# Optimization experiments

Measured on AMD Instinct MI355X. Metric: run time of the kernel, lower is better.

Reference implementation:

```python
import jax, jax.numpy as jnp
import numpy as np

STEPS = 16      # max ICP iterations (module init arg `steps`)
TOL = 1e-6      # convergence tolerance (module init arg `tol`)


def _sqdist(a, b):
    # a: [B,N,3], b: [B,M,3] -> squared Euclidean distances [B,N,M] via GEMM
    a2 = jnp.sum(a * a, axis=-1)            # [B,N]
    b2 = jnp.sum(b * b, axis=-1)            # [B,M]
    ab = jnp.einsum('bnd,bmd->bnm', a, b)   # [B,N,M]
    return jnp.maximum(a2[..., :, None] + b2[..., None, :] - 2.0 * ab, 0.0)


def _kabsch(src, tgt):
    # Rigid transform (R, t) minimizing ||R*src + t - tgt|| via 3x3 SVD (svdtf)
    cs = src.mean(axis=-2, keepdims=True)   # [B,1,3]
    ct = tgt.mean(axis=-2, keepdims=True)
    H = jnp.einsum('bni,bnj->bij', src - cs, tgt - ct)  # [B,3,3]
    U, S, Vt = jnp.linalg.svd(H)
    V = jnp.swapaxes(Vt, -1, -2)
    Ut = jnp.swapaxes(U, -1, -2)
    d = jnp.linalg.det(V @ Ut)              # [B], reflection fix
    D = (jnp.zeros_like(H)
         .at[..., 0, 0].set(1.0)
         .at[..., 1, 1].set(1.0)
         .at[..., 2, 2].set(d))
    R = V @ D @ Ut                          # [B,3,3]
    t = ct[..., 0, :] - jnp.einsum('bij,bj->bi', R, cs[..., 0, :])  # [B,3]
    return R, t


def _icp(source, target):
    B = source.shape[0]

    def step(carry, _):
        temporal, errlast, done = carry
        d2 = _sqdist(temporal, target)                      # [B,N,M]
        knnidx = jnp.argmin(d2, axis=-1)                    # [B,N] 1-NN indices
        knnd2 = jnp.take_along_axis(d2, knnidx[..., None], axis=-1)[..., 0]
        errnew = jnp.sqrt(knnd2).mean(axis=-1)              # [B]
        # early-exit: once all batch errors converged, freeze state (emulates break)
        done = done | jnp.all(jnp.abs(errnew - errlast) < TOL)
        knntgt = jnp.take_along_axis(target, knnidx[..., None], axis=-2)  # [B,N,3]
        R, t = _kabsch(temporal, knntgt)
        new_temporal = jnp.einsum('bij,bnj->bni', R, temporal) + t[:, None, :]
        temporal = jnp.where(done, temporal, new_temporal)
        errlast = jnp.where(done, errlast, errnew)
        return (temporal, errlast, done), None

    init = (source, jnp.zeros((B,), source.dtype), jnp.array(False))
    (temporal, _, _), _ = jax.lax.scan(step, init, None, length=STEPS)
    # final transform from original source to aligned cloud (svdtf(source, temporal))
    R, t = _kabsch(source, temporal)
    return jnp.concatenate([R, t[..., None]], axis=-1)    # [B,3,4] = [R | t]


def setup_inputs() -> dict:
    key = jax.random.key(0)
    k1, k2 = jax.random.split(key)
    source = jax.random.normal(k1, (4, 4096, 3), dtype=jnp.float32)
    target = jax.random.normal(k2, (4, 4096, 3), dtype=jnp.float32)
    return {"source": source, "target": target}


def reference(source, target):
    return _icp(source, target)
```

## Files before the change

### kernel.cpp

```cpp
#include <hip/hip_runtime.h>

#define BATCH   4
#define NPTS    4096
#define MPTS    4096
#define NSTEPS  16
#define ICP_TOL 1e-6f

#define TPB        512
#define NBLOCKS    256
#define BLK_PER_B  64

#define ACC_OFF 0
#define CNT_OFF 65536
#define MST_OFF 69632
#define ZERO_DWORDS ((CNT_OFF + 4096) / 4)

typedef float v2f __attribute__((ext_vector_type(2)));


__device__ inline void normalize3f(float v[3]) {
    float n2 = v[0]*v[0] + v[1]*v[1] + v[2]*v[2];
    float inv = (n2 > 1e-30f) ? (1.0f / sqrtf(n2)) : 0.0f;
    v[0] *= inv; v[1] *= inv; v[2] *= inv;
}

__device__ inline void cross3f(const float a[3], const float b[3], float c[3]) {
    c[0] = a[1]*b[2] - a[2]*b[1];
    c[1] = a[2]*b[0] - a[0]*b[2];
    c[2] = a[0]*b[1] - a[1]*b[0];
}

__device__ inline void eigvec_f32(const float K[3][3], float la, float lb, float v[3]) {
    float A[3][3], Bm[3][3], C[3][3];
    #pragma unroll
    for (int i = 0; i < 3; i++)
        #pragma unroll
        for (int j = 0; j < 3; j++) {
            A[i][j]  = K[i][j] - ((i == j) ? la : 0.0f);
            Bm[i][j] = K[i][j] - ((i == j) ? lb : 0.0f);
        }
    #pragma unroll
    for (int i = 0; i < 3; i++)
        #pragma unroll
        for (int j = 0; j < 3; j++) {
            float s = 0.0f;
            #pragma unroll
            for (int k = 0; k < 3; k++) s += A[i][k] * Bm[k][j];
            C[i][j] = s;
        }
    int best = 0; float bn = -1.0f;
    #pragma unroll
    for (int c = 0; c < 3; c++) {
        float n2 = C[0][c]*C[0][c] + C[1][c]*C[1][c] + C[2][c]*C[2][c];
        if (n2 > bn) { bn = n2; best = c; }
    }
    if (bn > 1e-28f) {
        float inv = 1.0f / sqrtf(bn);
        v[0] = C[0][best]*inv; v[1] = C[1][best]*inv; v[2] = C[2][best]*inv;
    } else {
        v[0] = 1.0f; v[1] = 0.0f; v[2] = 0.0f;
    }
}

__device__ inline void kabsch_f32(const double S[16], float R[3][3], float t[3]) {
    const double inv_n = 1.0 / (double)NPTS;
    float cs[3] = { (float)(S[0]*inv_n), (float)(S[1]*inv_n), (float)(S[2]*inv_n) };
    float ct[3] = { (float)(S[3]*inv_n), (float)(S[4]*inv_n), (float)(S[5]*inv_n) };
    float H[3][3];
    #pragma unroll
    for (int i = 0; i < 3; i++)
        #pragma unroll
        for (int j = 0; j < 3; j++)
            H[i][j] = (float)(S[6 + 3*i + j] - S[i]*S[3 + j]*inv_n);

    float K[3][3];
    #pragma unroll
    for (int i = 0; i < 3; i++)
        #pragma unroll
        for (int j = 0; j < 3; j++) {
            float s = 0.0f;
            #pragma unroll
            for (int k = 0; k < 3; k++) s += H[k][i]*H[k][j];
            K[i][j] = s;
        }

    float q = (K[0][0] + K[1][1] + K[2][2]) * (1.0f/3.0f);
    float p1 = K[0][1]*K[0][1] + K[0][2]*K[0][2] + K[1][2]*K[1][2];
    float a00 = K[0][0]-q, a11 = K[1][1]-q, a22 = K[2][2]-q;
    float p2 = a00*a00 + a11*a11 + a22*a22 + 2.0f*p1;
    float p = sqrtf(p2 * (1.0f/6.0f));
    float l1, l2, l3;
    if (p < 1e-18f) {
        l1 = l2 = l3 = q;
    } else {
        float ip = 1.0f / p;
        float b00 = a00*ip, b01 = K[0][1]*ip, b02 = K[0][2]*ip;
        float b11 = a11*ip, b12 = K[1][2]*ip, b22 = a22*ip;
        float detB = b00*(b11*b22 - b12*b12)
                   - b01*(b01*b22 - b12*b02)
                   + b02*(b01*b12 - b11*b02);
        float r = 0.5f * detB;
        r = fminf(fmaxf(r, -1.0f), 1.0f);
        float phi = acosf(r) * (1.0f/3.0f);
        l1 = q + 2.0f*p*cosf(phi);
        l3 = q + 2.0f*p*cosf(phi + 2.0943951f);
        l2 = 3.0f*q - l1 - l3;
    }

    float v1[3], v2[3], v3[3];
    eigvec_f32(K, l2, l3, v1);
    eigvec_f32(K, l1, l3, v2);
    float d12 = v1[0]*v2[0] + v1[1]*v2[1] + v1[2]*v2[2];
    #pragma unroll
    for (int i = 0; i < 3; i++) v2[i] -= d12*v1[i];
    normalize3f(v2);
    cross3f(v1, v2, v3);

    float u1[3], u2[3], u3[3];
    #pragma unroll
    for (int i = 0; i < 3; i++) u1[i] = H[i][0]*v1[0] + H[i][1]*v1[1] + H[i][2]*v1[2];
    normalize3f(u1);
    #pragma unroll
    for (int i = 0; i < 3; i++) u2[i] = H[i][0]*v2[0] + H[i][1]*v2[1] + H[i][2]*v2[2];
    float du = u1[0]*u2[0] + u1[1]*u2[1] + u1[2]*u2[2];
    #pragma unroll
    for (int i = 0; i < 3; i++) u2[i] -= du*u1[i];
    normalize3f(u2);
    cross3f(u1, u2, u3);

    #pragma unroll
    for (int i = 0; i < 3; i++)
        #pragma unroll
        for (int j = 0; j < 3; j++)
            R[i][j] = v1[i]*u1[j] + v2[i]*u2[j] + v3[i]*u3[j];
    #pragma unroll
    for (int i = 0; i < 3; i++)
        t[i] = ct[i] - (R[i][0]*cs[0] + R[i][1]*cs[1] + R[i][2]*cs[2]);
}


__global__ void k_init(unsigned int* __restrict__ wsz) {
    int i = blockIdx.x * blockDim.x + threadIdx.x;
    if (i < ZERO_DWORDS) wsz[i] = 0u;
}

__global__ __launch_bounds__(TPB, 2)
void k_icp(const float* __restrict__ src, const float* __restrict__ tgt,
           double* __restrict__ accD, unsigned int* __restrict__ cntU,
           float* __restrict__ MstF) {
    __shared__ __align__(16) float Xs[MPTS];
    __shared__ __align__(16) float Ys[MPTS];
    __shared__ __align__(16) float Zs[MPTS];
    __shared__ __align__(16) float Ws[MPTS];
    __shared__ double pmem[8][16];
    __shared__ double Ssh[16];
    __shared__ float  Rsh[14];

    const int bid  = blockIdx.x;
    const int b    = bid >> 6;
    const int lb   = bid & (BLK_PER_B - 1);
    const int tid  = threadIdx.x;
    const int w    = tid >> 6;
    const int lane = tid & 63;

    const float* tgb = tgt + (size_t)b * MPTS * 3;
    const float* spb = src + ((size_t)b * NPTS + lb * 64 + w * 8) * 3;

    for (int i = tid; i < MPTS; i += TPB) {
        float x = tgb[3*i], y = tgb[3*i+1], z = tgb[3*i+2];
        Xs[i] = x; Ys[i] = y; Zs[i] = z;
        Ws[i] = 0.5f*(x*x + y*y + z*z);
    }

    float px[8], py[8], pz[8];
    #pragma unroll
    for (int k = 0; k < 8; k++) {
        px[k] = spb[3*k+0]; py[k] = spb[3*k+1]; pz[k] = spb[3*k+2];
    }
    float m00=1.f,m01=0.f,m02=0.f, m10=0.f,m11=1.f,m12=0.f, m20=0.f,m21=0.f,m22=1.f;
    float mt0=0.f,mt1=0.f,mt2=0.f;
    __syncthreads();

    const v2f* Xv = (const v2f*)Xs;
    const v2f* Yv = (const v2f*)Ys;
    const v2f* Zv = (const v2f*)Zs;
    const v2f* Wv = (const v2f*)Ws;

    for (int s = 0; s < NSTEPS; ++s) {
        v2f nx[8], ny[8], nz[8];
        #pragma unroll
        for (int k = 0; k < 8; k++) {
            nx[k] = (v2f){-px[k], -px[k]};
            ny[k] = (v2f){-py[k], -py[k]};
            nz[k] = (v2f){-pz[k], -pz[k]};
        }
        float bs[8]; int bm[8];
        #pragma unroll
        for (int k = 0; k < 8; k++) { bs[k] = 1e30f; bm[k] = 0; }

        #pragma unroll 4
        for (int j = 0; j < (MPTS/2)/64; ++j) {
            int q = (j << 6) | lane;
            v2f Xp = Xv[q], Yp = Yv[q], Zp = Zv[q], Wp = Wv[q];
            #pragma unroll
            for (int k = 0; k < 8; k++) {
                v2f f0, f1, f2;
                asm("v_pk_fma_f32 %0, %1, %2, %3" : "=v"(f0) : "v"(nx[k]), "v"(Xp), "v"(Wp));
                asm("v_pk_fma_f32 %0, %1, %2, %3" : "=v"(f1) : "v"(ny[k]), "v"(Yp), "v"(f0));
                asm("v_pk_fma_f32 %0, %1, %2, %3" : "=v"(f2) : "v"(nz[k]), "v"(Zp), "v"(f1));
                float lo = f2.x, hi = f2.y;
                float bsn = fminf(fminf(lo, hi), bs[k]);
                int ip = (q << 1) | ((hi < lo) ? 1 : 0);
                bm[k] = (bsn < bs[k]) ? ip : bm[k];
                bs[k] = bsn;
            }
        }
        #pragma unroll
        for (int off = 32; off >= 1; off >>= 1) {
            #pragma unroll
            for (int k = 0; k < 8; k++) {
                float os = __shfl_xor(bs[k], off);
                int   om = __shfl_xor(bm[k], off);
                if (os < bs[k] || (os == bs[k] && om < bm[k])) { bs[k] = os; bm[k] = om; }
            }
        }
        if (lane == 0) {
            double acc[16];
            #pragma unroll
            for (int i = 0; i < 16; i++) acc[i] = 0.0;
            #pragma unroll
            for (int k = 0; k < 8; k++) {
                int mm = bm[k];
                float qx = Xs[mm], qy = Ys[mm], qz = Zs[mm];
                float a2 = px[k]*px[k] + py[k]*py[k] + pz[k]*pz[k];
                float d2 = fmaxf(a2 + 2.0f*bs[k], 0.0f);
                double pxd = px[k], pyd = py[k], pzd = pz[k];
                double qxd = qx, qyd = qy, qzd = qz;
                acc[0] += pxd;  acc[1] += pyd;  acc[2] += pzd;
                acc[3] += qxd;  acc[4] += qyd;  acc[5] += qzd;
                acc[6] += pxd*qxd;  acc[7]  += pxd*qyd;  acc[8]  += pxd*qzd;
                acc[9] += pyd*qxd;  acc[10] += pyd*qyd;  acc[11] += pyd*qzd;
                acc[12]+= pzd*qxd;  acc[13] += pzd*qyd;  acc[14] += pzd*qzd;
                acc[15]+= (double)sqrtf(d2);
            }
            #pragma unroll
            for (int i = 0; i < 16; i++) pmem[w][i] = acc[i];
        }
        __syncthreads();

        const int slot = (s * BATCH + b) * 16;
        if (w == 0) {
            if (lane < 16) {
                double v = pmem[0][lane] + pmem[1][lane] + pmem[2][lane] + pmem[3][lane]
                         + pmem[4][lane] + pmem[5][lane] + pmem[6][lane] + pmem[7][lane];
                unsafeAtomicAdd(&accD[(size_t)(slot + lane) * 8], v);
            }
            asm volatile("s_waitcnt vmcnt(0)" ::: "memory");
            if (lane == 0) {
                unsigned int* cp = &cntU[(size_t)(s * BATCH + b) * 16];
                __hip_atomic_fetch_add(cp, 1u, __ATOMIC_RELAXED, __HIP_MEMORY_SCOPE_AGENT);
                while (__hip_atomic_load(cp, __ATOMIC_ACQUIRE, __HIP_MEMORY_SCOPE_AGENT)
                       < (unsigned)BLK_PER_B)
                    __builtin_amdgcn_s_sleep(1);
            }
            if (lane < 16)
                Ssh[lane] = __hip_atomic_load(&accD[(size_t)(slot + lane) * 8],
                                              __ATOMIC_RELAXED, __HIP_MEMORY_SCOPE_AGENT);
            double S[16];
            #pragma unroll
            for (int i = 0; i < 16; i++) S[i] = Ssh[i];
            float R[3][3], t[3];
            kabsch_f32(S, R, t);
            if (lane == 0) {
                Rsh[0]=R[0][0]; Rsh[1]=R[0][1]; Rsh[2]=R[0][2];
                Rsh[3]=R[1][0]; Rsh[4]=R[1][1]; Rsh[5]=R[1][2];
                Rsh[6]=R[2][0]; Rsh[7]=R[2][1]; Rsh[8]=R[2][2];
                Rsh[9]=t[0];    Rsh[10]=t[1];   Rsh[11]=t[2];
                Rsh[12]=(float)(S[15] * (1.0 / (double)NPTS));
            }
        }
        __syncthreads();

        const float r00=Rsh[0], r01=Rsh[1], r02=Rsh[2];
        const float r10=Rsh[3], r11=Rsh[4], r12=Rsh[5];
        const float r20=Rsh[6], r21=Rsh[7], r22=Rsh[8];
        const float t0=Rsh[9], t1=Rsh[10], t2=Rsh[11];

        #pragma unroll
        for (int k = 0; k < 8; k++) {
            float x = px[k], y = py[k], z = pz[k];
            px[k] = r00*x + r01*y + r02*z + t0;
            py[k] = r10*x + r11*y + r12*z + t1;
            pz[k] = r20*x + r21*y + r22*z + t2;
        }
        float n00 = r00*m00 + r01*m10 + r02*m20;
        float n01 = r00*m01 + r01*m11 + r02*m21;
        float n02 = r00*m02 + r01*m12 + r02*m22;
        float n10 = r10*m00 + r11*m10 + r12*m20;
        float n11 = r10*m01 + r11*m11 + r12*m21;
        float n12 = r10*m02 + r11*m12 + r12*m22;
        float n20 = r20*m00 + r21*m10 + r22*m20;
        float n21 = r20*m01 + r21*m11 + r22*m21;
        float n22 = r20*m02 + r21*m12 + r22*m22;
        float nt0 = r00*mt0 + r01*mt1 + r02*mt2 + t0;
        float nt1 = r10*mt0 + r11*mt1 + r12*mt2 + t1;
        float nt2 = r20*mt0 + r21*mt1 + r22*mt2 + t2;
        m00=n00; m01=n01; m02=n02; m10=n10; m11=n11; m12=n12;
        m20=n20; m21=n21; m22=n22; mt0=nt0; mt1=nt1; mt2=nt2;

        if (lb == 0 && tid == 0) {
            float* o = MstF + (size_t)(s * BATCH + b) * 16;
            o[0] = Rsh[12];
            o[1] = m00; o[2] = m01; o[3] = m02;
            o[4] = m10; o[5] = m11; o[6] = m12;
            o[7] = m20; o[8] = m21; o[9] = m22;
            o[10] = mt0; o[11] = mt1; o[12] = mt2;
        }
    }
}

__global__ void k_final(const float* __restrict__ MstF, float* __restrict__ out) {
    const int lane = threadIdx.x;
    float ep0 = 0.f, ep1 = 0.f, ep2 = 0.f, ep3 = 0.f;
    int sel = NSTEPS - 1;
    bool ident = false;
    bool found = false;
    for (int s = 0; s < NSTEPS && !found; ++s) {
        float e0 = MstF[(s*4+0)*16], e1 = MstF[(s*4+1)*16];
        float e2 = MstF[(s*4+2)*16], e3 = MstF[(s*4+3)*16];
        if (fabsf(e0-ep0) < ICP_TOL && fabsf(e1-ep1) < ICP_TOL &&
            fabsf(e2-ep2) < ICP_TOL && fabsf(e3-ep3) < ICP_TOL) {
            found = true;
            if (s == 0) ident = true; else sel = s - 1;
        } else {
            ep0 = e0; ep1 = e1; ep2 = e2; ep3 = e3;
        }
    }
    if (lane < BATCH) {
        float* o = out + lane * 12;
        if (ident) {
            o[0]=1.f; o[1]=0.f; o[2]=0.f; o[3]=0.f;
            o[4]=0.f; o[5]=1.f; o[6]=0.f; o[7]=0.f;
            o[8]=0.f; o[9]=0.f; o[10]=1.f; o[11]=0.f;
        } else {
            const float* m = MstF + (size_t)(sel*4 + lane) * 16;
            o[0]=m[1];  o[1]=m[2];  o[2]=m[3];  o[3]=m[10];
            o[4]=m[4];  o[5]=m[5];  o[6]=m[6];  o[7]=m[11];
            o[8]=m[7];  o[9]=m[8];  o[10]=m[9]; o[11]=m[12];
        }
    }
}


extern "C" void kernel_launch(void* const* d_in, const int* in_sizes, int n_in,
                              void* d_out, int out_size, void* d_ws, size_t ws_size,
                              hipStream_t stream) {
    const float* src = (const float*)d_in[0];
    const float* tgt = (const float*)d_in[1];
    float* out = (float*)d_out;

    char* ws = (char*)d_ws;
    double*       accD = (double*)(ws + ACC_OFF);
    unsigned int* cntU = (unsigned int*)(ws + CNT_OFF);
    float*        MstF = (float*)(ws + MST_OFF);

    k_init<<<dim3((ZERO_DWORDS + 255)/256), dim3(256), 0, stream>>>((unsigned int*)ws);
    k_icp<<<dim3(NBLOCKS), dim3(TPB), 0, stream>>>(src, tgt, accD, cntU, MstF);
    k_final<<<dim3(1), dim3(64), 0, stream>>>(MstF, out);
}
```

Baseline: 418.8 us.

## Replace atomic-add grid barrier with per-block partial slots and flag polling

Each block now writes its 16 partial sums to its own slot and publishes a per-block step flag, instead of atomically adding into shared accumulators and bumping a shared counter. The wavefront polls all 64 flags of its batch in parallel, then reduces the 64 partials with a strided load and shuffle reduction. The partial buffers are double-buffered by step parity, and the init kernel now only zeroes 256 flag words. This targets contention on the atomic counter and the float64 atomics at each iteration's barrier. In exchange, every block redundantly reads all 64 partials, and reuse of the parity buffer relies on a block never getting two steps ahead of the others.

```diff
diff --git a/kernel.cpp b/kernel.cpp
--- a/kernel.cpp
+++ b/kernel.cpp
@@ -10,10 +10,10 @@
 #define NBLOCKS    256
 #define BLK_PER_B  64
 
-#define ACC_OFF 0
-#define CNT_OFF 65536
-#define MST_OFF 69632
-#define ZERO_DWORDS ((CNT_OFF + 4096) / 4)
+#define PART_OFF 0
+#define FLAG_OFF 65536
+#define MST_OFF  66560
+#define ZERO_DWORDS 256
 
 typedef float v2f __attribute__((ext_vector_type(2)));
 
@@ -139,14 +139,14 @@
 }
 
 
-__global__ void k_init(unsigned int* __restrict__ wsz) {
-    int i = blockIdx.x * blockDim.x + threadIdx.x;
-    if (i < ZERO_DWORDS) wsz[i] = 0u;
+__global__ void k_init(unsigned int* __restrict__ flagU) {
+    int i = threadIdx.x;
+    if (i < ZERO_DWORDS) flagU[i] = 0u;
 }
 
 __global__ __launch_bounds__(TPB, 2)
 void k_icp(const float* __restrict__ src, const float* __restrict__ tgt,
-           double* __restrict__ accD, unsigned int* __restrict__ cntU,
+           double* __restrict__ partD, unsigned int* __restrict__ flagU,
            float* __restrict__ MstF) {
     __shared__ __align__(16) float Xs[MPTS];
     __shared__ __align__(16) float Ys[MPTS];
@@ -185,6 +185,8 @@
     const v2f* Yv = (const v2f*)Ys;
     const v2f* Zv = (const v2f*)Zs;
     const v2f* Wv = (const v2f*)Ws;
+
+    unsigned int* flg_b = flagU + b * BLK_PER_B;
 
     for (int s = 0; s < NSTEPS; ++s) {
         v2f nx[8], ny[8], nz[8];
@@ -248,24 +250,37 @@
         }
         __syncthreads();
 
-        const int slot = (s * BATCH + b) * 16;
+        const int par = s & 1;
+        double* pslot = partD + ((size_t)(par * BATCH + b) * BLK_PER_B) * 16;
+
         if (w == 0) {
             if (lane < 16) {
                 double v = pmem[0][lane] + pmem[1][lane] + pmem[2][lane] + pmem[3][lane]
                          + pmem[4][lane] + pmem[5][lane] + pmem[6][lane] + pmem[7][lane];
-                unsafeAtomicAdd(&accD[(size_t)(slot + lane) * 8], v);
+                __hip_atomic_store(&pslot[(size_t)lb * 16 + lane], v,
+                                   __ATOMIC_RELAXED, __HIP_MEMORY_SCOPE_AGENT);
             }
             asm volatile("s_waitcnt vmcnt(0)" ::: "memory");
-            if (lane == 0) {
-                unsigned int* cp = &cntU[(size_t)(s * BATCH + b) * 16];
-                __hip_atomic_fetch_add(cp, 1u, __ATOMIC_RELAXED, __HIP_MEMORY_SCOPE_AGENT);
-                while (__hip_atomic_load(cp, __ATOMIC_ACQUIRE, __HIP_MEMORY_SCOPE_AGENT)
-                       < (unsigned)BLK_PER_B)
-                    __builtin_amdgcn_s_sleep(1);
-            }
-            if (lane < 16)
-                Ssh[lane] = __hip_atomic_load(&accD[(size_t)(slot + lane) * 8],
+            if (lane == 0)
+                __hip_atomic_store(&flg_b[lb], (unsigned)(s + 1),
+                                   __ATOMIC_RELAXED, __HIP_MEMORY_SCOPE_AGENT);
+            for (;;) {
+                unsigned f = __hip_atomic_load(&flg_b[lane],
+                                               __ATOMIC_RELAXED, __HIP_MEMORY_SCOPE_AGENT);
+                if (__all((int)(f >= (unsigned)(s + 1)))) break;
+                __builtin_amdgcn_s_sleep(1);
+            }
+            {
+                int v = lane & 15, c = lane >> 4;
+                double ssum = 0.0;
+                #pragma unroll
+                for (int r = 0; r < 16; r++)
+                    ssum += __hip_atomic_load(&pslot[(size_t)(c * 16 + r) * 16 + v],
                                               __ATOMIC_RELAXED, __HIP_MEMORY_SCOPE_AGENT);
+                ssum += __shfl_xor(ssum, 16);
+                ssum += __shfl_xor(ssum, 32);
+                if (lane < 16) Ssh[lane] = ssum;
+            }
             double S[16];
             #pragma unroll
             for (int i = 0; i < 16; i++) S[i] = Ssh[i];
@@ -360,11 +375,11 @@
     float* out = (float*)d_out;
 
     char* ws = (char*)d_ws;
-    double*       accD = (double*)(ws + ACC_OFF);
-    unsigned int* cntU = (unsigned int*)(ws + CNT_OFF);
-    float*        MstF = (float*)(ws + MST_OFF);
-
-    k_init<<<dim3((ZERO_DWORDS + 255)/256), dim3(256), 0, stream>>>((unsigned int*)ws);
-    k_icp<<<dim3(NBLOCKS), dim3(TPB), 0, stream>>>(src, tgt, accD, cntU, MstF);
+    double*       partD = (double*)(ws + PART_OFF);
+    unsigned int* flagU = (unsigned int*)(ws + FLAG_OFF);
+    float*        MstF  = (float*)(ws + MST_OFF);
+
+    k_init<<<dim3(1), dim3(ZERO_DWORDS), 0, stream>>>(flagU);
+    k_icp<<<dim3(NBLOCKS), dim3(TPB), 0, stream>>>(src, tgt, partD, flagU, MstF);
     k_final<<<dim3(1), dim3(64), 0, stream>>>(MstF, out);
 }
```

Measured after the change: 395.5 us. -5.6%, faster.
